# Kernel tuning notes

Hardware: AMD Instinct MI355X
Metric: run time of the kernel (lower is better)

The kernel has to match this reference:

```python
import jax, jax.numpy as jnp
import numpy as np

# --- static config (matches init_kwargs) ---
B, N, M = 128, 32, 32
C_IMG, NUM_HIDDEN, NUM_CLASSES = 1, 16, 3
INPUT_DIM = C_IMG + NUM_HIDDEN + NUM_CLASSES          # 20
OUT_DIM = NUM_HIDDEN + NUM_CLASSES + 2                # 21 (moving -> 2 action channels)
C_STATE = INPUT_DIM - C_IMG                           # 19
N_NEO, M_NEO = N - 2, M - 2                           # size_neo=None -> N-2
N_ACTIVE, M_ACTIVE = N - 2, M - 2
ITERATIONS = 10
IN_FEAT = 9 * INPUT_DIM + 2                           # 182, position='current'
THRESH = 0.0007


def setup_inputs() -> dict:
    key = jax.random.key(0)
    ks = jax.random.split(key, 7)
    images = jax.random.uniform(ks[0], (B, N, M, C_IMG), dtype=jnp.float32)
    W1 = jax.random.normal(ks[1], (IN_FEAT, 30), dtype=jnp.float32) * 0.08
    b1 = jnp.zeros((30,), jnp.float32)
    W2 = jax.random.normal(ks[2], (30, 30), dtype=jnp.float32) * 0.18
    b2 = jnp.zeros((30,), jnp.float32)
    W3 = jax.random.normal(ks[3], (30, OUT_DIM), dtype=jnp.float32) * 0.18
    b3 = jnp.zeros((OUT_DIM,), jnp.float32)
    return {"images": images, "W1": W1, "b1": b1, "W2": W2, "b2": b2, "W3": W3, "b3": b3}


def _custom_round(a):
    # positive -> +1, negative -> -1 (with deadzone |a| <= 0.0007 -> 0)
    return jnp.where(a > THRESH, 1, jnp.where(a < -THRESH, -1, 0)).astype(jnp.int32)


def _run(images, W1, b1, W2, b2, W3, b3):
    dx = jnp.arange(3)
    b_idx = jnp.arange(B)[:, None, None, None, None]        # (B,1,1,1,1)
    # fixed 3x3 windows into state (comms): state[x:x+3, y:y+3]
    sr = (jnp.arange(N_NEO)[:, None] + dx)[:, None, :, None]  # (Nn,1,3,1)
    sc = (jnp.arange(M_NEO)[:, None] + dx)[None, :, None, :]  # (1,Mn,1,3)
    half_n = N // 2
    half_m = M // 2

    # initial perception matrix: identity grid (N_neo == N_active)
    gx, gy = jnp.meshgrid(jnp.arange(N_NEO), jnp.arange(M_NEO), indexing="ij")
    perc0 = jnp.broadcast_to(jnp.stack([gx, gy], -1).astype(jnp.int32), (B, N_NEO, M_NEO, 2))
    state0 = jnp.zeros((B, N, M, C_STATE), jnp.float32)
    guesses0 = jnp.zeros((B * N_NEO * M_NEO, OUT_DIM), jnp.float32)

    def step(carry, _):
        state, perc, _ = carry
        px = perc[..., 0]  # (B,Nn,Mn) int32
        py = perc[..., 1]
        # dynamic 3x3 image patches at (px, py)
        rows = px[..., None, None] + dx[:, None]            # (B,Nn,Mn,3,1)
        cols = py[..., None, None] + dx[None, :]            # (B,Nn,Mn,1,3)
        perc_patch = images[b_idx, rows, cols, :]           # (B,Nn,Mn,3,3,C_IMG)
        comms = state[:, sr, sc, :]                          # (B,Nn,Mn,3,3,C_STATE)
        feat = jnp.concatenate([perc_patch, comms], axis=-1)  # (B,Nn,Mn,3,3,INPUT_DIM)
        feat = feat.reshape(B * N_NEO * M_NEO, 9 * INPUT_DIM)
        # position='current' features
        pos_x = ((px - half_n) / half_n).astype(jnp.float32).reshape(-1, 1)
        pos_y = ((py - half_m) / half_m).astype(jnp.float32).reshape(-1, 1)
        inp = jnp.concatenate([feat, pos_x, pos_y], axis=-1)  # (B*Nn*Mn, 182)
        h = jax.nn.relu(inp @ W1 + b1)
        h = jax.nn.relu(h @ W2 + b2)
        guesses = h @ W3 + b3                                 # (B*Nn*Mn, 21)
        outputs = guesses.reshape(B, N_NEO, M_NEO, OUT_DIM)
        state = state.at[:, 1:1 + N_NEO, 1:1 + M_NEO, :].add(outputs[..., :C_STATE])
        # movement: round actions to {-1,0,1}, add, clip to [0, N_active-1]
        delta = _custom_round(outputs[..., -2:])
        perc = jnp.clip(perc + delta, 0, N_ACTIVE - 1)
        return (state, perc, guesses), None

    (state, perc, guesses), _ = jax.lax.scan(step, (state0, perc0, guesses0), None, length=ITERATIONS)
    class_state = state[:, 1:1 + N_NEO, 1:1 + M_NEO, -NUM_CLASSES:]
    return class_state, guesses


def reference(images, W1, b1, W2, b2, W3, b3):
    return _run(images, W1, b1, W2, b2, W3, b3)
```

## Files before the change

kernel.cpp:

```cpp
#include <hip/hip_runtime.h>

#define B_      128
#define NPIX    32
#define NNEO    30
#define CPAD    20
#define OUTD    21
#define ITERS   10
#define THRESHV 0.0007f
#define HSTRIDE 31

#define STATE_ELEMS_PAD (B_ * NPIX * NPIX * CPAD)
#define NCELLS      (B_ * NNEO * NNEO)
#define CLASS_ELEMS (NCELLS * 3)

__global__ void nca_init(float* __restrict__ stateA, float* __restrict__ stateB) {
    int idx = blockIdx.x * blockDim.x + threadIdx.x;
    const int total = B_ * 124 * CPAD;
    if (idx >= total) return;
    int c  = idx % CPAD;
    int t2 = idx / CPAD;
    int cellp = t2 % 124;
    int b    = t2 / 124;
    int i, j;
    if (cellp < 32)      { i = 0;  j = cellp; }
    else if (cellp < 64) { i = 31; j = cellp - 32; }
    else { int k = cellp - 64; i = 1 + (k >> 1); j = (k & 1) ? 31 : 0; }
    size_t off = (((size_t)b * NPIX + i) * NPIX + j) * CPAD + c;
    stateA[off] = 0.0f;
    stateB[off] = 0.0f;
}


#define ROW15(A, x, wrp) do { const float xx_ = (x); \
    const float* __restrict__ w_ = (wrp); \
    _Pragma("unroll") for (int o_ = 0; o_ < 15; o_++) (A)[o_] += xx_ * w_[o_]; \
} while (0)

#define ROW12(A, x, wrp) do { const float xx_ = (x); \
    const float* __restrict__ w_ = (wrp); \
    _Pragma("unroll") for (int o_ = 0; o_ < 12; o_++) (A)[o_] += xx_ * w_[o_]; \
} while (0)

#define ROW9(A, x, wrp) do { const float xx_ = (x); \
    const float* __restrict__ w_ = (wrp); \
    _Pragma("unroll") for (int o_ = 0; o_ < 9; o_++) (A)[o_] += xx_ * w_[o_]; \
} while (0)

template<int MODE>
__global__ __launch_bounds__(512, 4)
void nca_step(const float* __restrict__ img,
              const float* __restrict__ W1, const float* __restrict__ b1,
              const float* __restrict__ W2, const float* __restrict__ b2,
              const float* __restrict__ W3, const float* __restrict__ b3,
              const float* __restrict__ state_old, float* __restrict__ state_new,
              int* perc, float* __restrict__ guesses_out,
              float* __restrict__ class_out)
{
    __shared__ float s_state[10 * NPIX * CPAD];
    __shared__ float s_img[NPIX * NPIX];
    __shared__ float s_h[256 * HSTRIDE];

    const int b   = blockIdx.y;
    const int rg  = blockIdx.x;
    const int i0  = rg * 8;
    const int nr  = (rg == 3) ? 6 : 8;
    const int tid = threadIdx.x;
    const int h   = __builtin_amdgcn_readfirstlane(tid >> 8);
    const int cell = tid & 255;
    const int qoff = h * 15;

    if (MODE != 0) {
        const int n4 = (nr + 2) * (NPIX * CPAD / 4);
        const float4* __restrict__ gs4 =
            (const float4*)(state_old + ((size_t)b * NPIX + i0) * (NPIX * CPAD));
        float4* s4 = (float4*)s_state;
        for (int t = tid; t < n4; t += 512) s4[t] = gs4[t];
    }
    if (tid < 256)
        ((float4*)s_img)[tid] = ((const float4*)(img + (size_t)b * NPIX * NPIX))[tid];
    __syncthreads();

    const int cells = nr * NNEO;
    const bool active = cell < cells;

    int r = 0, j = 0, i = 0, gcell = 0, px = 0, py = 0;
    if (active) {
        r = cell / NNEO;
        j = cell - r * NNEO;
        i = i0 + r;
        gcell = (b * NNEO + i) * NNEO + j;
        if (MODE == 0) { px = i; py = j; }
        else           { px = perc[2 * gcell]; py = perc[2 * gcell + 1]; }
    }

    float a1[15];
    {
        float acc[15];
#pragma unroll
        for (int o = 0; o < 15; o++) acc[o] = b1[qoff + o];
        if (active) {
            if (MODE == 0) {
#pragma clang loop unroll(disable)
                for (int pr = 0; pr < 3; pr++) {
#pragma clang loop unroll(disable)
                    for (int pc = 0; pc < 3; pc++) {
                        const float iv = s_img[(px + pr) * NPIX + (py + pc)];
                        ROW15(acc, iv, W1 + (pr * 3 + pc) * 600 + qoff);
                    }
                }
            } else {
#pragma clang loop unroll(disable)
                for (int pr = 0; pr < 3; pr++) {
#pragma clang loop unroll(disable)
                    for (int pc = 0; pc < 3; pc++) {
                        const float iv = s_img[(px + pr) * NPIX + (py + pc)];
                        const float* __restrict__ wp = W1 + (pr * 3 + pc) * 600 + qoff;
                        const float4* __restrict__ sp =
                            (const float4*)&s_state[((r + pr) * NPIX + (j + pc)) * CPAD];
                        const float4 ga = sp[0], gb = sp[1], gc = sp[2],
                                     gd = sp[3], ge = sp[4];
                        ROW15(acc, iv,   wp);
                        ROW15(acc, ga.x, wp + 30);  ROW15(acc, ga.y, wp + 60);
                        ROW15(acc, ga.z, wp + 90);  ROW15(acc, ga.w, wp + 120);
                        ROW15(acc, gb.x, wp + 150); ROW15(acc, gb.y, wp + 180);
                        ROW15(acc, gb.z, wp + 210); ROW15(acc, gb.w, wp + 240);
                        ROW15(acc, gc.x, wp + 270); ROW15(acc, gc.y, wp + 300);
                        ROW15(acc, gc.z, wp + 330); ROW15(acc, gc.w, wp + 360);
                        ROW15(acc, gd.x, wp + 390); ROW15(acc, gd.y, wp + 420);
                        ROW15(acc, gd.z, wp + 450); ROW15(acc, gd.w, wp + 480);
                        ROW15(acc, ge.x, wp + 510); ROW15(acc, ge.y, wp + 540);
                        ROW15(acc, ge.z, wp + 570);
                    }
                }
            }
            const float posx = (float)(px - 16) * 0.0625f;
            const float posy = (float)(py - 16) * 0.0625f;
            ROW15(acc, posx, W1 + 180 * 30 + qoff);
            ROW15(acc, posy, W1 + 181 * 30 + qoff);
        }
#pragma unroll
        for (int o = 0; o < 15; o++) a1[o] = fmaxf(acc[o], 0.0f);
        if (active) {
#pragma unroll
            for (int o = 0; o < 15; o++) s_h[cell * HSTRIDE + qoff + o] = a1[o];
        }
    }
    __syncthreads();

    float h2[15];
    {
        float acc[15];
#pragma unroll
        for (int o = 0; o < 15; o++) acc[o] = b2[qoff + o];
        if (active) {
            if (h == 0) {
#pragma unroll
                for (int k = 0; k < 15; k++)
                    ROW15(acc, a1[k], W2 + k * 30);
#pragma clang loop unroll(disable)
                for (int k = 15; k < 30; k++) {
                    const float x = s_h[cell * HSTRIDE + k];
                    ROW15(acc, x, W2 + k * 30);
                }
            } else {
#pragma clang loop unroll(disable)
                for (int k = 0; k < 15; k++) {
                    const float x = s_h[cell * HSTRIDE + k];
                    ROW15(acc, x, W2 + k * 30 + 15);
                }
#pragma unroll
                for (int k = 0; k < 15; k++)
                    ROW15(acc, a1[k], W2 + (k + 15) * 30 + 15);
            }
        }
#pragma unroll
        for (int o = 0; o < 15; o++) h2[o] = fmaxf(acc[o], 0.0f);
    }
    __syncthreads();
    if (active) {
#pragma unroll
        for (int o = 0; o < 15; o++) s_h[cell * HSTRIDE + qoff + o] = h2[o];
    }
    __syncthreads();

    if (active) {
        const size_t coff = (((size_t)b * NPIX + (i + 1)) * NPIX + (j + 1)) * CPAD;
        const int    lc   = ((r + 1) * NPIX + (j + 1)) * CPAD;
        if (h == 0) {
            float ov[12];
#pragma unroll
            for (int c = 0; c < 12; c++) ov[c] = b3[c];
#pragma unroll
            for (int k = 0; k < 15; k++)
                ROW12(ov, h2[k], W3 + k * 21);
#pragma clang loop unroll(disable)
            for (int k = 15; k < 30; k++) {
                const float x = s_h[cell * HSTRIDE + k];
                ROW12(ov, x, W3 + k * 21);
            }
            if (MODE == 2) {
                float* __restrict__ g = guesses_out + (size_t)gcell * OUTD;
#pragma unroll
                for (int c = 0; c < 12; c++) g[c] = ov[c];
            } else {
                float4* __restrict__ ns4 = (float4*)(state_new + coff);
                if (MODE == 0) {
                    ns4[0] = make_float4(ov[0], ov[1], ov[2],  ov[3]);
                    ns4[1] = make_float4(ov[4], ov[5], ov[6],  ov[7]);
                    ns4[2] = make_float4(ov[8], ov[9], ov[10], ov[11]);
                } else {
                    const float4* __restrict__ cs4 = (const float4*)&s_state[lc];
                    const float4 c0 = cs4[0], c1 = cs4[1], c2 = cs4[2];
                    ns4[0] = make_float4(c0.x + ov[0], c0.y + ov[1],
                                         c0.z + ov[2], c0.w + ov[3]);
                    ns4[1] = make_float4(c1.x + ov[4], c1.y + ov[5],
                                         c1.z + ov[6], c1.w + ov[7]);
                    ns4[2] = make_float4(c2.x + ov[8], c2.y + ov[9],
                                         c2.z + ov[10], c2.w + ov[11]);
                }
            }
        } else {
            float ov[9];
#pragma unroll
            for (int c = 0; c < 9; c++) ov[c] = b3[12 + c];
#pragma clang loop unroll(disable)
            for (int k = 0; k < 15; k++) {
                const float x = s_h[cell * HSTRIDE + k];
                ROW9(ov, x, W3 + k * 21 + 12);
            }
#pragma unroll
            for (int k = 0; k < 15; k++)
                ROW9(ov, h2[k], W3 + (k + 15) * 21 + 12);
            if (MODE == 2) {
                float* __restrict__ g = guesses_out + (size_t)gcell * OUTD;
#pragma unroll
                for (int c = 0; c < 9; c++) g[12 + c] = ov[c];
                const float4 c4 = *(const float4*)&s_state[lc + 16];
                float* __restrict__ cs = class_out + (size_t)gcell * 3;
                cs[0] = c4.x + ov[4];
                cs[1] = c4.y + ov[5];
                cs[2] = c4.z + ov[6];
            } else {
                float4* __restrict__ ns4 = (float4*)(state_new + coff);
                if (MODE == 0) {
                    ns4[3] = make_float4(ov[0], ov[1], ov[2], ov[3]);
                    ns4[4] = make_float4(ov[4], ov[5], ov[6], 0.0f);
                } else {
                    const float4 c3 = *(const float4*)&s_state[lc + 12];
                    const float4 c4 = *(const float4*)&s_state[lc + 16];
                    ns4[3] = make_float4(c3.x + ov[0], c3.y + ov[1],
                                         c3.z + ov[2], c3.w + ov[3]);
                    ns4[4] = make_float4(c4.x + ov[4], c4.y + ov[5],
                                         c4.z + ov[6], 0.0f);
                }
                int dxm = (ov[7] > THRESHV) ? 1 : ((ov[7] < -THRESHV) ? -1 : 0);
                int dym = (ov[8] > THRESHV) ? 1 : ((ov[8] < -THRESHV) ? -1 : 0);
                px += dxm; py += dym;
                px = (px < 0) ? 0 : ((px > NNEO - 1) ? NNEO - 1 : px);
                py = (py < 0) ? 0 : ((py > NNEO - 1) ? NNEO - 1 : py);
                perc[2 * gcell + 0] = px;
                perc[2 * gcell + 1] = py;
            }
        }
    }
}

extern "C" void kernel_launch(void* const* d_in, const int* in_sizes, int n_in,
                              void* d_out, int out_size, void* d_ws, size_t ws_size,
                              hipStream_t stream) {
    const float* img = (const float*)d_in[0];
    const float* W1  = (const float*)d_in[1];
    const float* b1  = (const float*)d_in[2];
    const float* W2  = (const float*)d_in[3];
    const float* b2  = (const float*)d_in[4];
    const float* W3  = (const float*)d_in[5];
    const float* b3  = (const float*)d_in[6];

    float* out = (float*)d_out;
    float* class_out   = out;
    float* guesses_out = out + CLASS_ELEMS;

    float* stateA = (float*)d_ws;
    float* stateB = stateA + STATE_ELEMS_PAD;
    int*   perc   = (int*)(stateB + STATE_ELEMS_PAD);

    {
        const int total = B_ * 124 * CPAD;
        nca_init<<<(total + 255) / 256, 256, 0, stream>>>(stateA, stateB);
    }

    const dim3 grid(4, B_);
    nca_step<0><<<grid, 512, 0, stream>>>(img, W1, b1, W2, b2, W3, b3,
                                          stateA, stateB, perc,
                                          guesses_out, class_out);
    for (int t = 1; t < ITERS - 1; t++) {
        const float* so = (t & 1) ? stateB : stateA;
        float*       sn = (t & 1) ? stateA : stateB;
        nca_step<1><<<grid, 512, 0, stream>>>(img, W1, b1, W2, b2, W3, b3,
                                              so, sn, perc,
                                              guesses_out, class_out);
    }
    nca_step<2><<<grid, 512, 0, stream>>>(img, W1, b1, W2, b2, W3, b3,
                                          stateB, stateA, perc,
                                          guesses_out, class_out);
}
```

Before: 336.4 us.

## Fuse all NCA iterations into one persistent kernel with halo exchange flags

```diff
diff --git a/kernel.cpp b/kernel.cpp
--- a/kernel.cpp
+++ b/kernel.cpp
@@ -9,26 +9,9 @@
 #define THRESHV 0.0007f
 #define HSTRIDE 31
 
-#define STATE_ELEMS_PAD (B_ * NPIX * NPIX * CPAD)
 #define NCELLS      (B_ * NNEO * NNEO)
 #define CLASS_ELEMS (NCELLS * 3)
-
-__global__ void nca_init(float* __restrict__ stateA, float* __restrict__ stateB) {
-    int idx = blockIdx.x * blockDim.x + threadIdx.x;
-    const int total = B_ * 124 * CPAD;
-    if (idx >= total) return;
-    int c  = idx % CPAD;
-    int t2 = idx / CPAD;
-    int cellp = t2 % 124;
-    int b    = t2 / 124;
-    int i, j;
-    if (cellp < 32)      { i = 0;  j = cellp; }
-    else if (cellp < 64) { i = 31; j = cellp - 32; }
-    else { int k = cellp - 64; i = 1 + (k >> 1); j = (k & 1) ? 31 : 0; }
-    size_t off = (((size_t)b * NPIX + i) * NPIX + j) * CPAD + c;
-    stateA[off] = 0.0f;
-    stateB[off] = 0.0f;
-}
+#define HALOROW     (NPIX * CPAD)
 
 
 #define ROW15(A, x, wrp) do { const float xx_ = (x); \
@@ -46,221 +29,242 @@
     _Pragma("unroll") for (int o_ = 0; o_ < 9; o_++) (A)[o_] += xx_ * w_[o_]; \
 } while (0)
 
-template<int MODE>
+__global__ void nca_zero_flags(int* __restrict__ flags) {
+    if (threadIdx.x < 512) flags[threadIdx.x] = 0;
+}
+
 __global__ __launch_bounds__(512, 4)
-void nca_step(const float* __restrict__ img,
-              const float* __restrict__ W1, const float* __restrict__ b1,
-              const float* __restrict__ W2, const float* __restrict__ b2,
-              const float* __restrict__ W3, const float* __restrict__ b3,
-              const float* __restrict__ state_old, float* __restrict__ state_new,
-              int* perc, float* __restrict__ guesses_out,
-              float* __restrict__ class_out)
+void nca_persist(const float* __restrict__ img,
+                 const float* __restrict__ W1, const float* __restrict__ b1,
+                 const float* __restrict__ W2, const float* __restrict__ b2,
+                 const float* __restrict__ W3, const float* __restrict__ b3,
+                 float* __restrict__ hbuf, int* __restrict__ flags,
+                 float* __restrict__ guesses_out, float* __restrict__ class_out)
 {
-    __shared__ float s_state[10 * NPIX * CPAD];
+    __shared__ float s_state[10 * HALOROW];
     __shared__ float s_img[NPIX * NPIX];
     __shared__ float s_h[256 * HSTRIDE];
-
-    const int b   = blockIdx.y;
-    const int rg  = blockIdx.x;
-    const int i0  = rg * 8;
-    const int nr  = (rg == 3) ? 6 : 8;
+    __shared__ int   s_perc[256][2];
+
+    const int bid = blockIdx.x;
+    const int b   = bid >> 2;
+    const int q   = bid & 3;
+    const int r0  = (q < 2) ? q * 8 : 16 + (q - 2) * 7;
+    const int nr  = (q < 2) ? 8 : 7;
     const int tid = threadIdx.x;
     const int h   = __builtin_amdgcn_readfirstlane(tid >> 8);
     const int cell = tid & 255;
     const int qoff = h * 15;
 
-    if (MODE != 0) {
-        const int n4 = (nr + 2) * (NPIX * CPAD / 4);
-        const float4* __restrict__ gs4 =
-            (const float4*)(state_old + ((size_t)b * NPIX + i0) * (NPIX * CPAD));
-        float4* s4 = (float4*)s_state;
-        for (int t = tid; t < n4; t += 512) s4[t] = gs4[t];
-    }
+    for (int t2 = tid; t2 < 10 * HALOROW; t2 += 512) s_state[t2] = 0.0f;
     if (tid < 256)
-        ((float4*)s_img)[tid] = ((const float4*)(img + (size_t)b * NPIX * NPIX))[tid];
-    __syncthreads();
+        ((float4*)s_img)[tid] =
+            ((const float4*)(img + (size_t)b * (NPIX * NPIX)))[tid];
 
     const int cells = nr * NNEO;
     const bool active = cell < cells;
-
-    int r = 0, j = 0, i = 0, gcell = 0, px = 0, py = 0;
-    if (active) {
-        r = cell / NNEO;
-        j = cell - r * NNEO;
-        i = i0 + r;
-        gcell = (b * NNEO + i) * NNEO + j;
-        if (MODE == 0) { px = i; py = j; }
-        else           { px = perc[2 * gcell]; py = perc[2 * gcell + 1]; }
-    }
-
-    float a1[15];
-    {
-        float acc[15];
-#pragma unroll
-        for (int o = 0; o < 15; o++) acc[o] = b1[qoff + o];
+    int r = 0, j = 0;
+    if (active) { r = cell / NNEO; j = cell - r * NNEO; }
+    const int i = r0 + r;
+    const int gcell = (b * NNEO + i) * NNEO + j;
+    int px = i, py = j;
+
+    float* __restrict__ myslot = hbuf + (size_t)bid * (4 * HALOROW);
+    const float* __restrict__ prevslot =
+        (q > 0) ? hbuf + (size_t)(bid - 1) * (4 * HALOROW) + 2 * HALOROW : nullptr;
+    const float* __restrict__ nextslot =
+        (q < 3) ? hbuf + (size_t)(bid + 1) * (4 * HALOROW) : nullptr;
+    int* pflag = (q > 0) ? flags + (bid - 1) : nullptr;
+    int* nflag = (q < 3) ? flags + (bid + 1) : nullptr;
+
+    __syncthreads();
+
+    for (int t = 0; t < ITERS; t++) {
+        if (t > 0) {
+            if (tid == 0) {
+                if (pflag)
+                    while (__hip_atomic_load(pflag, __ATOMIC_ACQUIRE,
+                                             __HIP_MEMORY_SCOPE_AGENT) < t)
+                        __builtin_amdgcn_s_sleep(16);
+                if (nflag)
+                    while (__hip_atomic_load(nflag, __ATOMIC_ACQUIRE,
+                                             __HIP_MEMORY_SCOPE_AGENT) < t)
+                        __builtin_amdgcn_s_sleep(16);
+            }
+            __syncthreads();
+            const int buf = (t - 1) & 1;
+            if (q > 0)
+                for (int t2 = tid; t2 < HALOROW; t2 += 512)
+                    s_state[t2] = prevslot[buf * HALOROW + t2];
+            if (q < 3)
+                for (int t2 = tid; t2 < HALOROW; t2 += 512)
+                    s_state[(nr + 1) * HALOROW + t2] =
+                        nextslot[buf * HALOROW + t2];
+            __syncthreads();
+            if (active) { px = s_perc[cell][0]; py = s_perc[cell][1]; }
+        }
+
+        float a1[15];
+        {
+            float acc[15];
+#pragma unroll
+            for (int o = 0; o < 15; o++) acc[o] = b1[qoff + o];
+            if (active) {
+                if (t == 0) {
+#pragma clang loop unroll(disable)
+                    for (int pr = 0; pr < 3; pr++) {
+#pragma clang loop unroll(disable)
+                        for (int pc = 0; pc < 3; pc++) {
+                            const float iv = s_img[(px + pr) * NPIX + (py + pc)];
+                            ROW15(acc, iv, W1 + (pr * 3 + pc) * 600 + qoff);
+                        }
+                    }
+                } else {
+#pragma clang loop unroll(disable)
+                    for (int pr = 0; pr < 3; pr++) {
+#pragma clang loop unroll(disable)
+                        for (int pc = 0; pc < 3; pc++) {
+                            const float iv = s_img[(px + pr) * NPIX + (py + pc)];
+                            const float* __restrict__ wp =
+                                W1 + (pr * 3 + pc) * 600 + qoff;
+                            const float4* __restrict__ sp = (const float4*)
+                                &s_state[((r + pr) * NPIX + (j + pc)) * CPAD];
+                            const float4 ga = sp[0], gb = sp[1], gc = sp[2],
+                                         gd = sp[3], ge = sp[4];
+                            ROW15(acc, iv,   wp);
+                            ROW15(acc, ga.x, wp + 30);  ROW15(acc, ga.y, wp + 60);
+                            ROW15(acc, ga.z, wp + 90);  ROW15(acc, ga.w, wp + 120);
+                            ROW15(acc, gb.x, wp + 150); ROW15(acc, gb.y, wp + 180);
+                            ROW15(acc, gb.z, wp + 210); ROW15(acc, gb.w, wp + 240);
+                            ROW15(acc, gc.x, wp + 270); ROW15(acc, gc.y, wp + 300);
+                            ROW15(acc, gc.z, wp + 330); ROW15(acc, gc.w, wp + 360);
+                            ROW15(acc, gd.x, wp + 390); ROW15(acc, gd.y, wp + 420);
+                            ROW15(acc, gd.z, wp + 450); ROW15(acc, gd.w, wp + 480);
+                            ROW15(acc, ge.x, wp + 510); ROW15(acc, ge.y, wp + 540);
+                            ROW15(acc, ge.z, wp + 570);
+                        }
+                    }
+                }
+                const float posx = (float)(px - 16) * 0.0625f;
+                const float posy = (float)(py - 16) * 0.0625f;
+                ROW15(acc, posx, W1 + 180 * 30 + qoff);
+                ROW15(acc, posy, W1 + 181 * 30 + qoff);
+            }
+#pragma unroll
+            for (int o = 0; o < 15; o++) a1[o] = fmaxf(acc[o], 0.0f);
+            if (active) {
+#pragma unroll
+                for (int o = 0; o < 15; o++)
+                    s_h[cell * HSTRIDE + qoff + o] = a1[o];
+            }
+        }
+        __syncthreads();
+
+        float h2[15];
+        {
+            float acc[15];
+#pragma unroll
+            for (int o = 0; o < 15; o++) acc[o] = b2[qoff + o];
+            if (active) {
+                if (h == 0) {
+#pragma unroll
+                    for (int k = 0; k < 15; k++)
+                        ROW15(acc, a1[k], W2 + k * 30);
+#pragma clang loop unroll(disable)
+                    for (int k = 15; k < 30; k++) {
+                        const float x = s_h[cell * HSTRIDE + k];
+                        ROW15(acc, x, W2 + k * 30);
+                    }
+                } else {
+#pragma clang loop unroll(disable)
+                    for (int k = 0; k < 15; k++) {
+                        const float x = s_h[cell * HSTRIDE + k];
+                        ROW15(acc, x, W2 + k * 30 + 15);
+                    }
+#pragma unroll
+                    for (int k = 0; k < 15; k++)
+                        ROW15(acc, a1[k], W2 + (k + 15) * 30 + 15);
+                }
+            }
+#pragma unroll
+            for (int o = 0; o < 15; o++) h2[o] = fmaxf(acc[o], 0.0f);
+        }
+        __syncthreads();
         if (active) {
-            if (MODE == 0) {
-#pragma clang loop unroll(disable)
-                for (int pr = 0; pr < 3; pr++) {
-#pragma clang loop unroll(disable)
-                    for (int pc = 0; pc < 3; pc++) {
-                        const float iv = s_img[(px + pr) * NPIX + (py + pc)];
-                        ROW15(acc, iv, W1 + (pr * 3 + pc) * 600 + qoff);
-                    }
-                }
-            } else {
-#pragma clang loop unroll(disable)
-                for (int pr = 0; pr < 3; pr++) {
-#pragma clang loop unroll(disable)
-                    for (int pc = 0; pc < 3; pc++) {
-                        const float iv = s_img[(px + pr) * NPIX + (py + pc)];
-                        const float* __restrict__ wp = W1 + (pr * 3 + pc) * 600 + qoff;
-                        const float4* __restrict__ sp =
-                            (const float4*)&s_state[((r + pr) * NPIX + (j + pc)) * CPAD];
-                        const float4 ga = sp[0], gb = sp[1], gc = sp[2],
-                                     gd = sp[3], ge = sp[4];
-                        ROW15(acc, iv,   wp);
-                        ROW15(acc, ga.x, wp + 30);  ROW15(acc, ga.y, wp + 60);
-                        ROW15(acc, ga.z, wp + 90);  ROW15(acc, ga.w, wp + 120);
-                        ROW15(acc, gb.x, wp + 150); ROW15(acc, gb.y, wp + 180);
-                        ROW15(acc, gb.z, wp + 210); ROW15(acc, gb.w, wp + 240);
-                        ROW15(acc, gc.x, wp + 270); ROW15(acc, gc.y, wp + 300);
-                        ROW15(acc, gc.z, wp + 330); ROW15(acc, gc.w, wp + 360);
-                        ROW15(acc, gd.x, wp + 390); ROW15(acc, gd.y, wp + 420);
-                        ROW15(acc, gd.z, wp + 450); ROW15(acc, gd.w, wp + 480);
-                        ROW15(acc, ge.x, wp + 510); ROW15(acc, ge.y, wp + 540);
-                        ROW15(acc, ge.z, wp + 570);
-                    }
-                }
-            }
-            const float posx = (float)(px - 16) * 0.0625f;
-            const float posy = (float)(py - 16) * 0.0625f;
-            ROW15(acc, posx, W1 + 180 * 30 + qoff);
-            ROW15(acc, posy, W1 + 181 * 30 + qoff);
-        }
-#pragma unroll
-        for (int o = 0; o < 15; o++) a1[o] = fmaxf(acc[o], 0.0f);
+#pragma unroll
+            for (int o = 0; o < 15; o++)
+                s_h[cell * HSTRIDE + qoff + o] = h2[o];
+        }
+        __syncthreads();
+
         if (active) {
-#pragma unroll
-            for (int o = 0; o < 15; o++) s_h[cell * HSTRIDE + qoff + o] = a1[o];
-        }
-    }
-    __syncthreads();
-
-    float h2[15];
-    {
-        float acc[15];
-#pragma unroll
-        for (int o = 0; o < 15; o++) acc[o] = b2[qoff + o];
-        if (active) {
+            const int lc = ((r + 1) * NPIX + (j + 1)) * CPAD;
             if (h == 0) {
+                float ov[12];
+#pragma unroll
+                for (int c = 0; c < 12; c++) ov[c] = b3[c];
 #pragma unroll
                 for (int k = 0; k < 15; k++)
-                    ROW15(acc, a1[k], W2 + k * 30);
+                    ROW12(ov, h2[k], W3 + k * 21);
 #pragma clang loop unroll(disable)
                 for (int k = 15; k < 30; k++) {
                     const float x = s_h[cell * HSTRIDE + k];
-                    ROW15(acc, x, W2 + k * 30);
+                    ROW12(ov, x, W3 + k * 21);
+                }
+                if (t == ITERS - 1) {
+                    float* __restrict__ g = guesses_out + (size_t)gcell * OUTD;
+#pragma unroll
+                    for (int c = 0; c < 12; c++) g[c] = ov[c];
+                } else {
+#pragma unroll
+                    for (int c = 0; c < 12; c++) s_state[lc + c] += ov[c];
                 }
             } else {
+                float ov[9];
+#pragma unroll
+                for (int c = 0; c < 9; c++) ov[c] = b3[12 + c];
 #pragma clang loop unroll(disable)
                 for (int k = 0; k < 15; k++) {
                     const float x = s_h[cell * HSTRIDE + k];
-                    ROW15(acc, x, W2 + k * 30 + 15);
+                    ROW9(ov, x, W3 + k * 21 + 12);
                 }
 #pragma unroll
                 for (int k = 0; k < 15; k++)
-                    ROW15(acc, a1[k], W2 + (k + 15) * 30 + 15);
-            }
-        }
-#pragma unroll
-        for (int o = 0; o < 15; o++) h2[o] = fmaxf(acc[o], 0.0f);
-    }
-    __syncthreads();
-    if (active) {
-#pragma unroll
-        for (int o = 0; o < 15; o++) s_h[cell * HSTRIDE + qoff + o] = h2[o];
-    }
-    __syncthreads();
-
-    if (active) {
-        const size_t coff = (((size_t)b * NPIX + (i + 1)) * NPIX + (j + 1)) * CPAD;
-        const int    lc   = ((r + 1) * NPIX + (j + 1)) * CPAD;
-        if (h == 0) {
-            float ov[12];
-#pragma unroll
-            for (int c = 0; c < 12; c++) ov[c] = b3[c];
-#pragma unroll
-            for (int k = 0; k < 15; k++)
-                ROW12(ov, h2[k], W3 + k * 21);
-#pragma clang loop unroll(disable)
-            for (int k = 15; k < 30; k++) {
-                const float x = s_h[cell * HSTRIDE + k];
-                ROW12(ov, x, W3 + k * 21);
-            }
-            if (MODE == 2) {
-                float* __restrict__ g = guesses_out + (size_t)gcell * OUTD;
-#pragma unroll
-                for (int c = 0; c < 12; c++) g[c] = ov[c];
-            } else {
-                float4* __restrict__ ns4 = (float4*)(state_new + coff);
-                if (MODE == 0) {
-                    ns4[0] = make_float4(ov[0], ov[1], ov[2],  ov[3]);
-                    ns4[1] = make_float4(ov[4], ov[5], ov[6],  ov[7]);
-                    ns4[2] = make_float4(ov[8], ov[9], ov[10], ov[11]);
-                } else {
-                    const float4* __restrict__ cs4 = (const float4*)&s_state[lc];
-                    const float4 c0 = cs4[0], c1 = cs4[1], c2 = cs4[2];
-                    ns4[0] = make_float4(c0.x + ov[0], c0.y + ov[1],
-                                         c0.z + ov[2], c0.w + ov[3]);
-                    ns4[1] = make_float4(c1.x + ov[4], c1.y + ov[5],
-                                         c1.z + ov[6], c1.w + ov[7]);
-                    ns4[2] = make_float4(c2.x + ov[8], c2.y + ov[9],
-                                         c2.z + ov[10], c2.w + ov[11]);
-                }
-            }
-        } else {
-            float ov[9];
-#pragma unroll
-            for (int c = 0; c < 9; c++) ov[c] = b3[12 + c];
-#pragma clang loop unroll(disable)
-            for (int k = 0; k < 15; k++) {
-                const float x = s_h[cell * HSTRIDE + k];
-                ROW9(ov, x, W3 + k * 21 + 12);
-            }
-#pragma unroll
-            for (int k = 0; k < 15; k++)
-                ROW9(ov, h2[k], W3 + (k + 15) * 21 + 12);
-            if (MODE == 2) {
-                float* __restrict__ g = guesses_out + (size_t)gcell * OUTD;
-#pragma unroll
-                for (int c = 0; c < 9; c++) g[12 + c] = ov[c];
-                const float4 c4 = *(const float4*)&s_state[lc + 16];
-                float* __restrict__ cs = class_out + (size_t)gcell * 3;
-                cs[0] = c4.x + ov[4];
-                cs[1] = c4.y + ov[5];
-                cs[2] = c4.z + ov[6];
-            } else {
-                float4* __restrict__ ns4 = (float4*)(state_new + coff);
-                if (MODE == 0) {
-                    ns4[3] = make_float4(ov[0], ov[1], ov[2], ov[3]);
-                    ns4[4] = make_float4(ov[4], ov[5], ov[6], 0.0f);
-                } else {
-                    const float4 c3 = *(const float4*)&s_state[lc + 12];
-                    const float4 c4 = *(const float4*)&s_state[lc + 16];
-                    ns4[3] = make_float4(c3.x + ov[0], c3.y + ov[1],
-                                         c3.z + ov[2], c3.w + ov[3]);
-                    ns4[4] = make_float4(c4.x + ov[4], c4.y + ov[5],
-                                         c4.z + ov[6], 0.0f);
-                }
-                int dxm = (ov[7] > THRESHV) ? 1 : ((ov[7] < -THRESHV) ? -1 : 0);
-                int dym = (ov[8] > THRESHV) ? 1 : ((ov[8] < -THRESHV) ? -1 : 0);
-                px += dxm; py += dym;
-                px = (px < 0) ? 0 : ((px > NNEO - 1) ? NNEO - 1 : px);
-                py = (py < 0) ? 0 : ((py > NNEO - 1) ? NNEO - 1 : py);
-                perc[2 * gcell + 0] = px;
-                perc[2 * gcell + 1] = py;
-            }
+                    ROW9(ov, h2[k], W3 + (k + 15) * 21 + 12);
+                if (t == ITERS - 1) {
+                    float* __restrict__ g = guesses_out + (size_t)gcell * OUTD;
+#pragma unroll
+                    for (int c = 0; c < 9; c++) g[12 + c] = ov[c];
+                    float* __restrict__ cs = class_out + (size_t)gcell * 3;
+#pragma unroll
+                    for (int cc = 0; cc < 3; cc++)
+                        cs[cc] = s_state[lc + 16 + cc] + ov[4 + cc];
+                } else {
+#pragma unroll
+                    for (int c = 0; c < 7; c++)
+                        s_state[lc + 12 + c] += ov[c];
+                    int dxm = (ov[7] > THRESHV) ? 1 : ((ov[7] < -THRESHV) ? -1 : 0);
+                    int dym = (ov[8] > THRESHV) ? 1 : ((ov[8] < -THRESHV) ? -1 : 0);
+                    px += dxm; py += dym;
+                    px = (px < 0) ? 0 : ((px > NNEO - 1) ? NNEO - 1 : px);
+                    py = (py < 0) ? 0 : ((py > NNEO - 1) ? NNEO - 1 : py);
+                    s_perc[cell][0] = px;
+                    s_perc[cell][1] = py;
+                }
+            }
+        }
+
+        if (t < ITERS - 1) {
+            __syncthreads();
+            const int buf = t & 1;
+            for (int t2 = tid; t2 < HALOROW; t2 += 512) {
+                myslot[buf * HALOROW + t2]               = s_state[HALOROW + t2];
+                myslot[(2 + buf) * HALOROW + t2] = s_state[nr * HALOROW + t2];
+            }
+            __syncthreads();
+            if (tid == 0)
+                __hip_atomic_store(flags + bid, t + 1, __ATOMIC_RELEASE,
+                                   __HIP_MEMORY_SCOPE_AGENT);
         }
     }
 }
@@ -280,27 +284,12 @@
     float* class_out   = out;
     float* guesses_out = out + CLASS_ELEMS;
 
-    float* stateA = (float*)d_ws;
-    float* stateB = stateA + STATE_ELEMS_PAD;
-    int*   perc   = (int*)(stateB + STATE_ELEMS_PAD);
-
-    {
-        const int total = B_ * 124 * CPAD;
-        nca_init<<<(total + 255) / 256, 256, 0, stream>>>(stateA, stateB);
-    }
-
-    const dim3 grid(4, B_);
-    nca_step<0><<<grid, 512, 0, stream>>>(img, W1, b1, W2, b2, W3, b3,
-                                          stateA, stateB, perc,
-                                          guesses_out, class_out);
-    for (int t = 1; t < ITERS - 1; t++) {
-        const float* so = (t & 1) ? stateB : stateA;
-        float*       sn = (t & 1) ? stateA : stateB;
-        nca_step<1><<<grid, 512, 0, stream>>>(img, W1, b1, W2, b2, W3, b3,
-                                              so, sn, perc,
-                                              guesses_out, class_out);
-    }
-    nca_step<2><<<grid, 512, 0, stream>>>(img, W1, b1, W2, b2, W3, b3,
-                                          stateB, stateA, perc,
-                                          guesses_out, class_out);
+    float* hbuf  = (float*)d_ws;
+    int*   flags = (int*)(hbuf + 512 * 4 * HALOROW);
+
+    nca_zero_flags<<<1, 512, 0, stream>>>(flags);
+
+    nca_persist<<<512, 512, 0, stream>>>(img, W1, b1, W2, b2, W3, b3,
+                                         hbuf, flags,
+                                         guesses_out, class_out);
 }
```

New measurement: 616.8 us. 1.83x slower.
